# Performance work log

Measured on AMD Instinct MI355X. Metric: run time of the kernel, lower is better.

The kernel has to match this reference:

```python
import jax, jax.numpy as jnp
import numpy as np
from jax import lax

R = 8
SCALE = 1.0          # alpha / r with alpha == r
RESCALE = 1.0        # rescale_factor computed at init (constant)
PAD, DIL, GROUPS, K = 1, 1, 1, 3
BS, CIN, COUT, L = 128, 64, 64, 8192
EMB, HID = 256, 256
BN_EPS = 1e-5


def _mlp(x, w1, b1, g, beta, w2, b2):
    # Linear -> BatchNorm1d(eval, running mean=0, var=1) -> GELU(exact) -> Linear
    h = x @ w1.T + b1
    h = h * (g / np.float32(np.sqrt(1.0 + BN_EPS))) + beta
    h = jax.nn.gelu(h, approximate=False)
    return h @ w2.T + b2


def _conv1d(x, w, groups):
    # x: [N, C, L], w: [O, C/groups, K]
    return lax.conv_general_dilated(
        x, w, window_strides=(1,), padding=[(PAD, PAD)], rhs_dilation=(DIL,),
        dimension_numbers=("NCH", "OIH", "NCH"), feature_group_count=groups)


def setup_inputs() -> dict:
    key = jax.random.key(0)
    ks = jax.random.split(key, 20)
    n = lambda i, shape, s=1.0: (jax.random.normal(ks[i], shape, dtype=jnp.float32) * s)
    return {
        "X": n(0, (BS, CIN, L)),
        "a_embedding": n(1, (BS, EMB)),
        "b_embedding": n(2, (BS, EMB)),
        "A_w1": n(3, (HID, EMB), 0.06), "A_b1": n(4, (HID,), 0.02),
        "A_bn_g": 1.0 + n(5, (HID,), 0.05), "A_bn_b": n(6, (HID,), 0.02),
        "A_w2": n(7, (CIN * R // GROUPS, HID), 0.06), "A_b2": n(8, (CIN * R // GROUPS,), 0.02),
        "B_w1": n(9, (HID, EMB), 0.06), "B_b1": n(10, (HID,), 0.02),
        "B_bn_g": 1.0 + n(11, (HID,), 0.05), "B_bn_b": n(12, (HID,), 0.02),
        "B_w2": n(13, (COUT * R * K, HID), 0.06), "B_b2": n(14, (COUT * R * K,), 0.02),
        "base_w": n(15, (COUT, CIN // GROUPS, K), 0.08), "base_b": n(16, (COUT,), 0.02),
    }


def reference(X, a_embedding, b_embedding,
              A_w1, A_b1, A_bn_g, A_bn_b, A_w2, A_b2,
              B_w1, B_b1, B_bn_g, B_bn_b, B_w2, B_b2,
              base_w, base_b):
    bs = X.shape[0]
    # rescale applied under no_grad in the original -> inputs carry no grad
    a = lax.stop_gradient(a_embedding * RESCALE)
    b = lax.stop_gradient(b_embedding * RESCALE)
    # per-sample low-rank factors
    A = _mlp(a, A_w1, A_b1, A_bn_g, A_bn_b, A_w2, A_b2).reshape(bs, CIN // GROUPS, R)
    B = _mlp(b, B_w1, B_b1, B_bn_g, B_bn_b, B_w2, B_b2).reshape(bs, R, COUT * K)
    # dynamic conv weight: bmm(A, B) -> [bs, Cin/g, Cout, K] -> [bs, Cout, Cin/g, K]
    W = jnp.einsum("bir,brm->bim", A, B).reshape(bs, CIN // GROUPS, COUT, K)
    W = jnp.transpose(W, (0, 2, 1, 3))  # [bs, Cout, Cin/g, K]
    # per-sample conv (equivalent to F.conv1d with groups=bs*groups trick)
    lora = jax.vmap(lambda x, w: _conv1d(x[None], w, GROUPS)[0])(X, W)  # [bs, Cout, L]
    base = _conv1d(X, base_w, GROUPS) + base_b[None, :, None]
    return lora * SCALE + base
```

## Files before the change

### kernel.cpp

```cpp
#include <hip/hip_runtime.h>
#include <hip/hip_bf16.h>

#define BS    128
#define NCIN  64
#define NCOUT 64
#define LLEN  8192
#define NK    3
#define NR    8
#define NEMB  256
#define NHID  256
#define WPS   (NCOUT * NCIN * NK)
#define NT    256

typedef __attribute__((ext_vector_type(4)))  float  f32x4;
typedef __attribute__((ext_vector_type(16))) float  f32x16;
typedef __attribute__((ext_vector_type(8)))  __bf16 bf16x8;

__device__ float  g_A[BS * 512];
__device__ float  g_B[BS * 1536];
__device__ __bf16 g_Wb[BS * WPS];

__global__ __launch_bounds__(256) void mlp_kernel(
    const float* __restrict__ a_emb, const float* __restrict__ b_emb,
    const float* __restrict__ A_w1, const float* __restrict__ A_b1,
    const float* __restrict__ A_g,  const float* __restrict__ A_beta,
    const float* __restrict__ A_w2, const float* __restrict__ A_b2,
    const float* __restrict__ B_w1, const float* __restrict__ B_b1,
    const float* __restrict__ B_g,  const float* __restrict__ B_beta,
    const float* __restrict__ B_w2, const float* __restrict__ B_b2)
{
    __shared__ __align__(16) float emb_s[NEMB];
    __shared__ __align__(16) float h_s[NHID];

    const int t      = threadIdx.x;
    const int branch = blockIdx.x >> 7;
    const int b      = blockIdx.x & 127;

    const float* emb  = (branch ? b_emb : a_emb) + (size_t)b * NEMB;
    const float* w1   = branch ? B_w1 : A_w1;
    const float* b1   = branch ? B_b1 : A_b1;
    const float* gg   = branch ? B_g  : A_g;
    const float* bt   = branch ? B_beta : A_beta;
    const float* w2   = branch ? B_w2 : A_w2;
    const float* b2   = branch ? B_b2 : A_b2;
    float* outp       = (branch ? g_B : g_A) + (size_t)b * (branch ? 1536 : 512);
    const int nloops  = branch ? 6 : 2;

    emb_s[t] = emb[t];
    __syncthreads();

    {
        float acc = b1[t];
        const f32x4* wr = (const f32x4*)(w1 + (size_t)t * NEMB);
        const f32x4* es = (const f32x4*)emb_s;
        for (int e = 0; e < NEMB / 4; ++e) {
            f32x4 w = wr[e], a = es[e];
            acc += w[0]*a[0] + w[1]*a[1] + w[2]*a[2] + w[3]*a[3];
        }
        float h = acc * (gg[t] * (1.0f / sqrtf(1.0f + 1e-5f))) + bt[t];
        h = 0.5f * h * (1.0f + erff(h * 0.70710678118654752f));
        h_s[t] = h;
    }
    __syncthreads();

    for (int oo = 0; oo < nloops; ++oo) {
        const int o = oo * 256 + t;
        float acc = b2[o];
        const f32x4* wr = (const f32x4*)(w2 + (size_t)o * NHID);
        const f32x4* hs = (const f32x4*)h_s;
        for (int e = 0; e < NHID / 4; ++e) {
            f32x4 w = wr[e], h = hs[e];
            acc += w[0]*h[0] + w[1]*h[1] + w[2]*h[2] + w[3]*h[3];
        }
        outp[o] = acc;
    }
}

__global__ __launch_bounds__(256) void assemble_kernel(const float* __restrict__ base_w)
{
    const int b  = blockIdx.x >> 2;
    const int q  = blockIdx.x & 3;
    const int t  = threadIdx.x;
    const int ci = t & 63;

    float Ar[NR];
    const f32x4* Ap = (const f32x4*)(g_A + (size_t)b * 512 + ci * NR);
    f32x4 a0 = Ap[0], a1 = Ap[1];
    Ar[0]=a0[0]; Ar[1]=a0[1]; Ar[2]=a0[2]; Ar[3]=a0[3];
    Ar[4]=a1[0]; Ar[5]=a1[1]; Ar[6]=a1[2]; Ar[7]=a1[3];

    const float* Bp = g_B + (size_t)b * 1536;
    for (int i = 0; i < 12; ++i) {
        const int w  = q * 3072 + i * 256 + t;
        const int k  = w >> 12;
        const int co = (w >> 6) & 63;
        float v = base_w[(size_t)(co * 64 + ci) * 3 + k];
        #pragma unroll
        for (int r = 0; r < NR; ++r) v += Ar[r] * Bp[r * 192 + co * 3 + k];
        g_Wb[(size_t)b * WPS + w] = (__bf16)v;
    }
}

__global__ __launch_bounds__(256) void conv_kernel(
    const float* __restrict__ X, const float* __restrict__ base_b,
    float* __restrict__ out)
{
    __shared__ __align__(16) unsigned char smem[33024];
    __bf16* xt = (__bf16*)smem;
    float*  ot = (float*)smem;

    const int t     = threadIdx.x;
    const int b     = blockIdx.x >> 5;
    const int tile  = blockIdx.x & 31;
    const int l0    = tile * NT;
    const int lane  = t & 63;
    const int wave  = t >> 6;
    const int l31   = lane & 31;
    const int khalf = lane >> 5;
    const int wco   = wave >> 1;
    const int wl    = wave & 1;

    {
        const int lb = t & 31;
        const int cb = t >> 5;
        f32x4 v[8][2];
        const float* xb = X + (size_t)b * NCIN * LLEN + l0 + lb * 8;
        #pragma unroll
        for (int c = 0; c < 8; ++c) {
            const float* xr = xb + (size_t)(cb * 8 + c) * LLEN;
            v[c][0] = *(const f32x4*)(xr);
            v[c][1] = *(const f32x4*)(xr + 4);
        }
        #pragma unroll
        for (int j = 0; j < 8; ++j) {
            const int lp = lb * 8 + j + 1;
            bf16x8 w;
            #pragma unroll
            for (int c = 0; c < 8; ++c) w[c] = (__bf16)v[c][j >> 2][j & 3];
            const int blk = cb ^ (lp & 7) ^ ((lp >> 3) & 7);
            *(bf16x8*)(xt + lp * 64 + blk * 8) = w;
        }
    }
    if (t < 128) {
        const int ci    = t & 63;
        const int right = t >> 6;
        const int gl    = right ? (l0 + NT) : (l0 - 1);
        const int lp    = right ? (NT + 1) : 0;
        const float v   = (gl >= 0 && gl < LLEN) ? X[(size_t)(b * NCIN + ci) * LLEN + gl] : 0.0f;
        const int blk   = (ci >> 3) ^ (lp & 7) ^ ((lp >> 3) & 7);
        xt[lp * 64 + blk * 8 + (ci & 7)] = (__bf16)v;
    }
    __syncthreads();

    bf16x8 af[3][4];
    {
        const __bf16* wb = g_Wb + (size_t)b * WPS + (wco * 32 + l31) * 64 + khalf * 8;
        #pragma unroll
        for (int tap = 0; tap < 3; ++tap)
            #pragma unroll
            for (int c16 = 0; c16 < 4; ++c16)
                af[tap][c16] = *(const bf16x8*)(wb + tap * 4096 + c16 * 16);
    }

    f32x16 acc[4] = {};
    #pragma unroll
    for (int tap = 0; tap < 3; ++tap) {
        #pragma unroll
        for (int c16 = 0; c16 < 4; ++c16) {
            #pragma unroll
            for (int n = 0; n < 4; ++n) {
                const int R   = wl * 128 + n * 32 + l31 + tap;
                const int blk = (c16 * 2 + khalf) ^ (R & 7) ^ ((R >> 3) & 7);
                bf16x8 bfr = *(const bf16x8*)(xt + R * 64 + blk * 8);
                acc[n] = __builtin_amdgcn_mfma_f32_32x32x16_bf16(af[tap][c16], bfr, acc[n], 0, 0, 0);
            }
        }
    }

    #pragma unroll
    for (int m = 0; m < 2; ++m) {
        __syncthreads();
        if (wco == m) {
            #pragma unroll
            for (int reg = 0; reg < 16; ++reg) {
                const int row = (reg & 3) + 8 * (reg >> 2) + 4 * khalf;
                const float bb = base_b[m * 32 + row];
                #pragma unroll
                for (int n = 0; n < 4; ++n)
                    ot[row * 258 + wl * 128 + n * 32 + l31] = acc[n][reg] + bb;
            }
        }
        __syncthreads();
        #pragma unroll
        for (int it = 0; it < 8; ++it) {
            const int c   = t + it * 256;
            const int co2 = c >> 6;
            const int lr4 = c & 63;
            f32x4 v = *(const f32x4*)(ot + co2 * 258 + lr4 * 4);
            const int co = m * 32 + co2;
            *(f32x4*)(out + (size_t)(b * NCOUT + co) * LLEN + l0 + lr4 * 4) = v;
        }
    }
}

extern "C" void kernel_launch(void* const* d_in, const int* in_sizes, int n_in,
                              void* d_out, int out_size, void* d_ws, size_t ws_size,
                              hipStream_t stream)
{
    const float* X      = (const float*)d_in[0];
    const float* a_emb  = (const float*)d_in[1];
    const float* b_emb  = (const float*)d_in[2];
    const float* A_w1   = (const float*)d_in[3];
    const float* A_b1   = (const float*)d_in[4];
    const float* A_g    = (const float*)d_in[5];
    const float* A_beta = (const float*)d_in[6];
    const float* A_w2   = (const float*)d_in[7];
    const float* A_b2   = (const float*)d_in[8];
    const float* B_w1   = (const float*)d_in[9];
    const float* B_b1   = (const float*)d_in[10];
    const float* B_g    = (const float*)d_in[11];
    const float* B_beta = (const float*)d_in[12];
    const float* B_w2   = (const float*)d_in[13];
    const float* B_b2   = (const float*)d_in[14];
    const float* base_w = (const float*)d_in[15];
    const float* base_b = (const float*)d_in[16];

    float* out = (float*)d_out;

    mlp_kernel<<<2 * BS, 256, 0, stream>>>(a_emb, b_emb,
        A_w1, A_b1, A_g, A_beta, A_w2, A_b2,
        B_w1, B_b1, B_g, B_beta, B_w2, B_b2);

    assemble_kernel<<<4 * BS, 256, 0, stream>>>(base_w);

    conv_kernel<<<BS * (LLEN / NT), 256, 0, stream>>>(X, base_b, out);
}
```

Before: 203.6 us.

## Make conv kernel persistent over L tiles with double-buffered prefetch; split MLP

The conv kernel now runs one block per (batch, quarter of L) and loops over 8 tiles. It loads the per-sample weight fragments and bias once, then prefetches the next X tile into registers while computing the current one into a double-buffered LDS area. Output is written straight from the MFMA accumulators instead of being staged through LDS, so each warp writes rows in 32-float segments rather than coalesced 16-byte vectors. The MLP is split into a hidden-layer kernel and an output-layer kernel with 8x more blocks, which adds parallelism at the cost of one extra launch and a global round trip for the hidden activations.

Measured after the change: 218.4 us. +7.3%, slower.

```diff
diff --git a/kernel.cpp b/kernel.cpp
--- a/kernel.cpp
+++ b/kernel.cpp
@@ -11,69 +11,78 @@
 #define NHID  256
 #define WPS   (NCOUT * NCIN * NK)
 #define NT    256
+#define NTILE 8
 
 typedef __attribute__((ext_vector_type(4)))  float  f32x4;
 typedef __attribute__((ext_vector_type(16))) float  f32x16;
 typedef __attribute__((ext_vector_type(8)))  __bf16 bf16x8;
 
+__device__ float  g_h[2][BS * NHID];
 __device__ float  g_A[BS * 512];
 __device__ float  g_B[BS * 1536];
 __device__ __bf16 g_Wb[BS * WPS];
 
-__global__ __launch_bounds__(256) void mlp_kernel(
+__global__ __launch_bounds__(256) void mlp_hid(
     const float* __restrict__ a_emb, const float* __restrict__ b_emb,
     const float* __restrict__ A_w1, const float* __restrict__ A_b1,
     const float* __restrict__ A_g,  const float* __restrict__ A_beta,
-    const float* __restrict__ A_w2, const float* __restrict__ A_b2,
     const float* __restrict__ B_w1, const float* __restrict__ B_b1,
-    const float* __restrict__ B_g,  const float* __restrict__ B_beta,
-    const float* __restrict__ B_w2, const float* __restrict__ B_b2)
+    const float* __restrict__ B_g,  const float* __restrict__ B_beta)
 {
     __shared__ __align__(16) float emb_s[NEMB];
-    __shared__ __align__(16) float h_s[NHID];
 
     const int t      = threadIdx.x;
     const int branch = blockIdx.x >> 7;
     const int b      = blockIdx.x & 127;
 
-    const float* emb  = (branch ? b_emb : a_emb) + (size_t)b * NEMB;
-    const float* w1   = branch ? B_w1 : A_w1;
-    const float* b1   = branch ? B_b1 : A_b1;
-    const float* gg   = branch ? B_g  : A_g;
-    const float* bt   = branch ? B_beta : A_beta;
-    const float* w2   = branch ? B_w2 : A_w2;
-    const float* b2   = branch ? B_b2 : A_b2;
-    float* outp       = (branch ? g_B : g_A) + (size_t)b * (branch ? 1536 : 512);
-    const int nloops  = branch ? 6 : 2;
+    const float* emb = (branch ? b_emb : a_emb) + (size_t)b * NEMB;
+    const float* w1  = branch ? B_w1 : A_w1;
+    const float* b1  = branch ? B_b1 : A_b1;
+    const float* gg  = branch ? B_g  : A_g;
+    const float* bt  = branch ? B_beta : A_beta;
 
     emb_s[t] = emb[t];
     __syncthreads();
 
-    {
-        float acc = b1[t];
-        const f32x4* wr = (const f32x4*)(w1 + (size_t)t * NEMB);
-        const f32x4* es = (const f32x4*)emb_s;
-        for (int e = 0; e < NEMB / 4; ++e) {
-            f32x4 w = wr[e], a = es[e];
-            acc += w[0]*a[0] + w[1]*a[1] + w[2]*a[2] + w[3]*a[3];
-        }
-        float h = acc * (gg[t] * (1.0f / sqrtf(1.0f + 1e-5f))) + bt[t];
-        h = 0.5f * h * (1.0f + erff(h * 0.70710678118654752f));
-        h_s[t] = h;
-    }
+    float acc = b1[t];
+    const f32x4* wr = (const f32x4*)(w1 + (size_t)t * NEMB);
+    const f32x4* es = (const f32x4*)emb_s;
+    for (int e = 0; e < NEMB / 4; ++e) {
+        f32x4 w = wr[e], a = es[e];
+        acc += w[0]*a[0] + w[1]*a[1] + w[2]*a[2] + w[3]*a[3];
+    }
+    float h = acc * (gg[t] * (1.0f / sqrtf(1.0f + 1e-5f))) + bt[t];
+    h = 0.5f * h * (1.0f + erff(h * 0.70710678118654752f));
+    g_h[branch][(size_t)b * NHID + t] = h;
+}
+
+__global__ __launch_bounds__(256) void mlp_out(
+    const float* __restrict__ A_w2, const float* __restrict__ A_b2,
+    const float* __restrict__ B_w2, const float* __restrict__ B_b2)
+{
+    __shared__ __align__(16) float h_s[NHID];
+
+    const int t      = threadIdx.x;
+    const int b      = blockIdx.x >> 3;
+    const int oo     = blockIdx.x & 7;
+    const int branch = (oo >= 2) ? 1 : 0;
+
+    h_s[t] = g_h[branch][(size_t)b * NHID + t];
     __syncthreads();
 
-    for (int oo = 0; oo < nloops; ++oo) {
-        const int o = oo * 256 + t;
-        float acc = b2[o];
-        const f32x4* wr = (const f32x4*)(w2 + (size_t)o * NHID);
-        const f32x4* hs = (const f32x4*)h_s;
-        for (int e = 0; e < NHID / 4; ++e) {
-            f32x4 w = wr[e], h = hs[e];
-            acc += w[0]*h[0] + w[1]*h[1] + w[2]*h[2] + w[3]*h[3];
-        }
-        outp[o] = acc;
-    }
+    const int o = branch ? (oo - 2) * 256 + t : oo * 256 + t;
+    const float* w2 = branch ? B_w2 : A_w2;
+    const float* b2 = branch ? B_b2 : A_b2;
+
+    float acc = b2[o];
+    const f32x4* wr = (const f32x4*)(w2 + (size_t)o * NHID);
+    const f32x4* hs = (const f32x4*)h_s;
+    for (int e = 0; e < NHID / 4; ++e) {
+        f32x4 w = wr[e], h = hs[e];
+        acc += w[0]*h[0] + w[1]*h[1] + w[2]*h[2] + w[3]*h[3];
+    }
+    if (branch) g_B[(size_t)b * 1536 + o] = acc;
+    else        g_A[(size_t)b * 512  + o] = acc;
 }
 
 __global__ __launch_bounds__(256) void assemble_kernel(const float* __restrict__ base_w)
@@ -101,36 +110,60 @@
     }
 }
 
-__global__ __launch_bounds__(256) void conv_kernel(
+__global__ __launch_bounds__(256, 2) void conv_kernel(
     const float* __restrict__ X, const float* __restrict__ base_b,
     float* __restrict__ out)
 {
-    __shared__ __align__(16) unsigned char smem[33024];
-    __bf16* xt = (__bf16*)smem;
-    float*  ot = (float*)smem;
+    __shared__ __align__(16) __bf16 xts[2][(NT + 2) * 64];
 
     const int t     = threadIdx.x;
-    const int b     = blockIdx.x >> 5;
-    const int tile  = blockIdx.x & 31;
-    const int l0    = tile * NT;
+    const int b     = blockIdx.x >> 2;
+    const int chunk = blockIdx.x & 3;
     const int lane  = t & 63;
     const int wave  = t >> 6;
     const int l31   = lane & 31;
     const int khalf = lane >> 5;
     const int wco   = wave >> 1;
     const int wl    = wave & 1;
-
+    const int lb    = t & 31;
+    const int cb    = t >> 5;
+
+    const float* xbase = X + (size_t)b * NCIN * LLEN;
+
+    bf16x8 af[3][4];
     {
-        const int lb = t & 31;
-        const int cb = t >> 5;
-        f32x4 v[8][2];
-        const float* xb = X + (size_t)b * NCIN * LLEN + l0 + lb * 8;
+        const __bf16* wb = g_Wb + (size_t)b * WPS + (wco * 32 + l31) * 64 + khalf * 8;
+        #pragma unroll
+        for (int tap = 0; tap < 3; ++tap)
+            #pragma unroll
+            for (int c16 = 0; c16 < 4; ++c16)
+                af[tap][c16] = *(const bf16x8*)(wb + tap * 4096 + c16 * 16);
+    }
+    float bb_reg[16];
+    #pragma unroll
+    for (int reg = 0; reg < 16; ++reg)
+        bb_reg[reg] = base_b[wco * 32 + (reg & 3) + 8 * (reg >> 2) + 4 * khalf];
+
+    f32x4 v[8][2];
+    float hv = 0.0f;
+
+    auto prefetch = [&](int lt) {
+        const float* xb = xbase + lt + lb * 8;
         #pragma unroll
         for (int c = 0; c < 8; ++c) {
             const float* xr = xb + (size_t)(cb * 8 + c) * LLEN;
             v[c][0] = *(const f32x4*)(xr);
             v[c][1] = *(const f32x4*)(xr + 4);
         }
+        if (t < 128) {
+            const int ci    = t & 63;
+            const int right = t >> 6;
+            const int gl    = right ? (lt + NT) : (lt - 1);
+            hv = (gl >= 0 && gl < LLEN) ? xbase[(size_t)ci * LLEN + gl] : 0.0f;
+        }
+    };
+    auto dswrite = [&](int p) {
+        __bf16* xp = xts[p];
         #pragma unroll
         for (int j = 0; j < 8; ++j) {
             const int lp = lb * 8 + j + 1;
@@ -138,68 +171,52 @@
             #pragma unroll
             for (int c = 0; c < 8; ++c) w[c] = (__bf16)v[c][j >> 2][j & 3];
             const int blk = cb ^ (lp & 7) ^ ((lp >> 3) & 7);
-            *(bf16x8*)(xt + lp * 64 + blk * 8) = w;
-        }
-    }
-    if (t < 128) {
-        const int ci    = t & 63;
-        const int right = t >> 6;
-        const int gl    = right ? (l0 + NT) : (l0 - 1);
-        const int lp    = right ? (NT + 1) : 0;
-        const float v   = (gl >= 0 && gl < LLEN) ? X[(size_t)(b * NCIN + ci) * LLEN + gl] : 0.0f;
-        const int blk   = (ci >> 3) ^ (lp & 7) ^ ((lp >> 3) & 7);
-        xt[lp * 64 + blk * 8 + (ci & 7)] = (__bf16)v;
-    }
+            *(bf16x8*)(xp + lp * 64 + blk * 8) = w;
+        }
+        if (t < 128) {
+            const int ci  = t & 63;
+            const int lp  = (t >> 6) ? (NT + 1) : 0;
+            const int blk = (ci >> 3) ^ (lp & 7) ^ ((lp >> 3) & 7);
+            xp[lp * 64 + blk * 8 + (ci & 7)] = (__bf16)hv;
+        }
+    };
+
+    const int l0 = chunk * (NT * NTILE);
+    prefetch(l0);
+    dswrite(0);
     __syncthreads();
 
-    bf16x8 af[3][4];
-    {
-        const __bf16* wb = g_Wb + (size_t)b * WPS + (wco * 32 + l31) * 64 + khalf * 8;
+    int p = 0;
+    for (int tt = 0; tt < NTILE; ++tt) {
+        const int lt = l0 + tt * NT;
+        if (tt < NTILE - 1) prefetch(lt + NT);
+
+        const __bf16* xp = xts[p];
+        f32x16 acc[4] = {};
         #pragma unroll
         for (int tap = 0; tap < 3; ++tap)
             #pragma unroll
             for (int c16 = 0; c16 < 4; ++c16)
-                af[tap][c16] = *(const bf16x8*)(wb + tap * 4096 + c16 * 16);
-    }
-
-    f32x16 acc[4] = {};
-    #pragma unroll
-    for (int tap = 0; tap < 3; ++tap) {
-        #pragma unroll
-        for (int c16 = 0; c16 < 4; ++c16) {
-            #pragma unroll
-            for (int n = 0; n < 4; ++n) {
-                const int R   = wl * 128 + n * 32 + l31 + tap;
-                const int blk = (c16 * 2 + khalf) ^ (R & 7) ^ ((R >> 3) & 7);
-                bf16x8 bfr = *(const bf16x8*)(xt + R * 64 + blk * 8);
-                acc[n] = __builtin_amdgcn_mfma_f32_32x32x16_bf16(af[tap][c16], bfr, acc[n], 0, 0, 0);
-            }
-        }
-    }
-
-    #pragma unroll
-    for (int m = 0; m < 2; ++m) {
+                #pragma unroll
+                for (int n = 0; n < 4; ++n) {
+                    const int R   = wl * 128 + n * 32 + l31 + tap;
+                    const int blk = (c16 * 2 + khalf) ^ (R & 7) ^ ((R >> 3) & 7);
+                    bf16x8 bfr = *(const bf16x8*)(xp + R * 64 + blk * 8);
+                    acc[n] = __builtin_amdgcn_mfma_f32_32x32x16_bf16(af[tap][c16], bfr, acc[n], 0, 0, 0);
+                }
+
+        #pragma unroll
+        for (int reg = 0; reg < 16; ++reg) {
+            const int co = wco * 32 + (reg & 3) + 8 * (reg >> 2) + 4 * khalf;
+            float* op = out + (size_t)(b * NCOUT + co) * LLEN + lt + wl * 128 + l31;
+            #pragma unroll
+            for (int n = 0; n < 4; ++n)
+                op[n * 32] = acc[n][reg] + bb_reg[reg];
+        }
+
+        if (tt < NTILE - 1) dswrite(p ^ 1);
         __syncthreads();
-        if (wco == m) {
-            #pragma unroll
-            for (int reg = 0; reg < 16; ++reg) {
-                const int row = (reg & 3) + 8 * (reg >> 2) + 4 * khalf;
-                const float bb = base_b[m * 32 + row];
-                #pragma unroll
-                for (int n = 0; n < 4; ++n)
-                    ot[row * 258 + wl * 128 + n * 32 + l31] = acc[n][reg] + bb;
-            }
-        }
-        __syncthreads();
-        #pragma unroll
-        for (int it = 0; it < 8; ++it) {
-            const int c   = t + it * 256;
-            const int co2 = c >> 6;
-            const int lr4 = c & 63;
-            f32x4 v = *(const f32x4*)(ot + co2 * 258 + lr4 * 4);
-            const int co = m * 32 + co2;
-            *(f32x4*)(out + (size_t)(b * NCOUT + co) * LLEN + l0 + lr4 * 4) = v;
-        }
+        p ^= 1;
     }
 }
 
@@ -227,11 +244,12 @@
 
     float* out = (float*)d_out;
 
-    mlp_kernel<<<2 * BS, 256, 0, stream>>>(a_emb, b_emb,
-        A_w1, A_b1, A_g, A_beta, A_w2, A_b2,
-        B_w1, B_b1, B_g, B_beta, B_w2, B_b2);
+    mlp_hid<<<2 * BS, 256, 0, stream>>>(a_emb, b_emb,
+        A_w1, A_b1, A_g, A_beta, B_w1, B_b1, B_g, B_beta);
+
+    mlp_out<<<8 * BS, 256, 0, stream>>>(A_w2, A_b2, B_w2, B_b2);
 
     assemble_kernel<<<4 * BS, 256, 0, stream>>>(base_w);
 
-    conv_kernel<<<BS * (LLEN / NT), 256, 0, stream>>>(X, base_b, out);
-}
+    conv_kernel<<<4 * BS, 256, 0, stream>>>(X, base_b, out);
+}
```

## Halve conv tile, drop LDS output staging, swizzle block order

Applied to the files above, without the earlier changes.

Reduces the conv tile from 256 to 128 positions, which doubles the grid to 8192 blocks and shrinks shared memory so more blocks can be resident (launch bounds now request 4). The output is written straight from the MFMA accumulators to global memory instead of going through an LDS transpose with extra barriers. Block indices are remapped so consecutive blocks spread across batches. The direct stores are 4-byte accesses that are less well coalesced than the earlier float4 stores, and the smaller tile increases the relative cost of halo loads and the per-block weight fragment loads.

Measured after the change: 221.0 us. 8.5% more time.

```diff
diff --git a/kernel.cpp b/kernel.cpp
--- a/kernel.cpp
+++ b/kernel.cpp
@@ -10,10 +10,11 @@
 #define NEMB  256
 #define NHID  256
 #define WPS   (NCOUT * NCIN * NK)
-#define NT    256
+#define NT    128
 
 typedef __attribute__((ext_vector_type(4)))  float  f32x4;
 typedef __attribute__((ext_vector_type(16))) float  f32x16;
+typedef __attribute__((ext_vector_type(4)))  __bf16 bf16x4;
 typedef __attribute__((ext_vector_type(8)))  __bf16 bf16x8;
 
 __device__ float  g_A[BS * 512];
@@ -101,54 +102,56 @@
     }
 }
 
-__global__ __launch_bounds__(256) void conv_kernel(
+__global__ __launch_bounds__(256, 4) void conv_kernel(
     const float* __restrict__ X, const float* __restrict__ base_b,
     float* __restrict__ out)
 {
-    __shared__ __align__(16) unsigned char smem[33024];
-    __bf16* xt = (__bf16*)smem;
-    float*  ot = (float*)smem;
+    __shared__ __align__(16) __bf16 xt[(NT + 2) * 64];
+
+    const int swz  = (blockIdx.x & 7) * 1024 + (blockIdx.x >> 3);
+    const int b    = swz >> 6;
+    const int tile = swz & 63;
+    const int l0   = tile * NT;
 
     const int t     = threadIdx.x;
-    const int b     = blockIdx.x >> 5;
-    const int tile  = blockIdx.x & 31;
-    const int l0    = tile * NT;
     const int lane  = t & 63;
     const int wave  = t >> 6;
     const int l31   = lane & 31;
     const int khalf = lane >> 5;
     const int wco   = wave >> 1;
     const int wl    = wave & 1;
+    const int lb    = t & 15;
+    const int cb    = t >> 4;
+
+    const float* xbase = X + (size_t)b * NCIN * LLEN;
 
     {
-        const int lb = t & 31;
-        const int cb = t >> 5;
-        f32x4 v[8][2];
-        const float* xb = X + (size_t)b * NCIN * LLEN + l0 + lb * 8;
-        #pragma unroll
-        for (int c = 0; c < 8; ++c) {
-            const float* xr = xb + (size_t)(cb * 8 + c) * LLEN;
+        f32x4 v[4][2];
+        const float* xb = xbase + l0 + lb * 8;
+        #pragma unroll
+        for (int c = 0; c < 4; ++c) {
+            const float* xr = xb + (size_t)(cb * 4 + c) * LLEN;
             v[c][0] = *(const f32x4*)(xr);
             v[c][1] = *(const f32x4*)(xr + 4);
         }
         #pragma unroll
         for (int j = 0; j < 8; ++j) {
             const int lp = lb * 8 + j + 1;
-            bf16x8 w;
+            bf16x4 w;
             #pragma unroll
-            for (int c = 0; c < 8; ++c) w[c] = (__bf16)v[c][j >> 2][j & 3];
-            const int blk = cb ^ (lp & 7) ^ ((lp >> 3) & 7);
-            *(bf16x8*)(xt + lp * 64 + blk * 8) = w;
-        }
-    }
-    if (t < 128) {
-        const int ci    = t & 63;
-        const int right = t >> 6;
-        const int gl    = right ? (l0 + NT) : (l0 - 1);
-        const int lp    = right ? (NT + 1) : 0;
-        const float v   = (gl >= 0 && gl < LLEN) ? X[(size_t)(b * NCIN + ci) * LLEN + gl] : 0.0f;
-        const int blk   = (ci >> 3) ^ (lp & 7) ^ ((lp >> 3) & 7);
-        xt[lp * 64 + blk * 8 + (ci & 7)] = (__bf16)v;
+            for (int c = 0; c < 4; ++c) w[c] = (__bf16)v[c][j >> 2][j & 3];
+            const int blk = (cb >> 1) ^ (lp & 7) ^ ((lp >> 3) & 7);
+            *(bf16x4*)(xt + lp * 64 + blk * 8 + (cb & 1) * 4) = w;
+        }
+        if (t < 128) {
+            const int ci    = t & 63;
+            const int right = t >> 6;
+            const int gl    = right ? (l0 + NT) : (l0 - 1);
+            const int lp    = right ? (NT + 1) : 0;
+            const float hv  = (gl >= 0 && gl < LLEN) ? xbase[(size_t)ci * LLEN + gl] : 0.0f;
+            const int blk   = (ci >> 3) ^ (lp & 7) ^ ((lp >> 3) & 7);
+            xt[lp * 64 + blk * 8 + (ci & 7)] = (__bf16)hv;
+        }
     }
     __syncthreads();
 
@@ -162,44 +165,28 @@
                 af[tap][c16] = *(const bf16x8*)(wb + tap * 4096 + c16 * 16);
     }
 
-    f32x16 acc[4] = {};
+    f32x16 acc[2] = {};
     #pragma unroll
-    for (int tap = 0; tap < 3; ++tap) {
-        #pragma unroll
-        for (int c16 = 0; c16 < 4; ++c16) {
+    for (int tap = 0; tap < 3; ++tap)
+        #pragma unroll
+        for (int c16 = 0; c16 < 4; ++c16)
             #pragma unroll
-            for (int n = 0; n < 4; ++n) {
-                const int R   = wl * 128 + n * 32 + l31 + tap;
+            for (int n = 0; n < 2; ++n) {
+                const int R   = wl * 64 + n * 32 + l31 + tap;
                 const int blk = (c16 * 2 + khalf) ^ (R & 7) ^ ((R >> 3) & 7);
                 bf16x8 bfr = *(const bf16x8*)(xt + R * 64 + blk * 8);
                 acc[n] = __builtin_amdgcn_mfma_f32_32x32x16_bf16(af[tap][c16], bfr, acc[n], 0, 0, 0);
             }
-        }
-    }
 
     #pragma unroll
-    for (int m = 0; m < 2; ++m) {
-        __syncthreads();
-        if (wco == m) {
-            #pragma unroll
-            for (int reg = 0; reg < 16; ++reg) {
-                const int row = (reg & 3) + 8 * (reg >> 2) + 4 * khalf;
-                const float bb = base_b[m * 32 + row];
-                #pragma unroll
-                for (int n = 0; n < 4; ++n)
-                    ot[row * 258 + wl * 128 + n * 32 + l31] = acc[n][reg] + bb;
-            }
-        }
-        __syncthreads();
-        #pragma unroll
-        for (int it = 0; it < 8; ++it) {
-            const int c   = t + it * 256;
-            const int co2 = c >> 6;
-            const int lr4 = c & 63;
-            f32x4 v = *(const f32x4*)(ot + co2 * 258 + lr4 * 4);
-            const int co = m * 32 + co2;
-            *(f32x4*)(out + (size_t)(b * NCOUT + co) * LLEN + l0 + lr4 * 4) = v;
-        }
+    for (int reg = 0; reg < 16; ++reg) {
+        const int col = (reg & 3) + 8 * (reg >> 2) + 4 * khalf;
+        const int co  = wco * 32 + col;
+        const float bb = base_b[co];
+        float* op = out + (size_t)(b * NCOUT + co) * LLEN + l0 + wl * 64 + l31;
+        #pragma unroll
+        for (int n = 0; n < 2; ++n)
+            op[n * 32] = acc[n][reg] + bb;
     }
 }
 
@@ -233,5 +220,5 @@
 
     assemble_kernel<<<4 * BS, 256, 0, stream>>>(base_w);
 
-    conv_kernel<<<BS * (LLEN / NT), 256, 0, stream>>>(X, base_b, out);
-}
+    conv_kernel<<<8192, 256, 0, stream>>>(X, base_b, out);
+}
```
